# Optimization experiments

Hardware: AMD Instinct MI355X
Metric: run time of the kernel (lower is better)

The kernel has to match this reference:

```python
import jax, jax.numpy as jnp
import numpy as np

B, V, C, CD, D, H, W = 1, 3, 32, 8, 32, 128, 160
LAMB = 1.5


def _bilinear(img, x, y):
    # img: [c, Hs, Ws]; x, y: pixel coords [D, HW]; zero padding, align_corners=True semantics
    c, Hs, Ws = img.shape
    x0 = jnp.floor(x)
    y0 = jnp.floor(y)
    x0i = x0.astype(jnp.int32)
    y0i = y0.astype(jnp.int32)
    wx = x - x0
    wy = y - y0
    imgf = img.reshape(c, Hs * Ws)

    def gather(xi, yi, w):
        valid = (xi >= 0) & (xi < Ws) & (yi >= 0) & (yi < Hs)
        lin = jnp.clip(yi, 0, Hs - 1) * Ws + jnp.clip(xi, 0, Ws - 1)
        v = jnp.take(imgf, lin.reshape(-1), axis=1).reshape((c,) + xi.shape)
        return v * (w * valid.astype(w.dtype))[None]

    return (gather(x0i, y0i, (1 - wx) * (1 - wy))
            + gather(x0i + 1, y0i, wx * (1 - wy))
            + gather(x0i, y0i + 1, (1 - wx) * wy)
            + gather(x0i + 1, y0i + 1, wx * wy))


def _homo_warp(src_fea, src_proj, ref_proj, depth_values):
    # src_fea [B,c,Hs,Ws]; projs [B,4,4]; depth_values [B,D,H,W] -> [B,c,D,H,W]
    b, c, Hs, Ws = src_fea.shape
    _, d, h, w = depth_values.shape
    proj = jnp.einsum('bij,bjk->bik', src_proj, jnp.linalg.inv(ref_proj))
    rot = proj[:, :3, :3]
    tr = proj[:, :3, 3]
    ys, xs = jnp.meshgrid(jnp.arange(h, dtype=src_fea.dtype), jnp.arange(w, dtype=src_fea.dtype), indexing='ij')
    xyz = jnp.stack([xs.reshape(-1), ys.reshape(-1), jnp.ones(h * w, dtype=src_fea.dtype)], 0)  # [3,HW]
    rx = jnp.einsum('bij,jn->bin', rot, xyz)  # [B,3,HW]
    dvals = depth_values.reshape(b, 1, d, h * w)
    pxyz = rx[:, :, None, :] * dvals + tr[:, :, None, None]  # [B,3,D,HW]
    z = pxyz[:, 2]
    px = pxyz[:, 0] / z  # [B,D,HW]
    py = pxyz[:, 1] / z
    out = jax.vmap(_bilinear)(src_fea, px, py)  # [B,c,D,HW]
    return out.reshape(b, c, d, h, w)


def setup_inputs() -> dict:
    key = jax.random.key(0)
    k1, k2, k3 = jax.random.split(key, 3)
    features = jax.random.normal(k1, (V, B, C, H, W), jnp.float32)
    deps_feature_stage = jax.random.normal(k2, (V, B, CD, H, W), jnp.float32)
    reg_w = jax.random.normal(k3, (1, C + CD), jnp.float32) * 0.1
    K = np.array([[200., 0., W / 2.], [0., 200., H / 2.], [0., 0., 1.]])
    mats = []
    for tx in [0.0, 1.0, -1.0]:
        Rt = np.eye(4)
        Rt[0, 3] = tx
        P = np.eye(4)
        P[:3, :4] = K @ Rt[:3, :4]
        mats.append(P)
    proj_matrices = jnp.asarray(np.stack(mats)[None], jnp.float32)  # [B,V,4,4]
    depth_values = jnp.broadcast_to(
        jnp.linspace(5.0, 10.0, D, dtype=jnp.float32)[None, :, None, None], (B, D, H, W)) + jnp.zeros((B, D, H, W), jnp.float32)
    return {'features': features, 'deps_feature_stage': deps_feature_stage,
            'proj_matrices': proj_matrices, 'depth_values': depth_values,
            'reg_w': reg_w, 'num_depth': D, 'stage_idx': 0}


def reference(features, deps_feature_stage, proj_matrices, depth_values, reg_w, num_depth, stage_idx):
    num_views = features.shape[0]
    d = depth_values.shape[1]
    ref_proj = proj_matrices[:, 0]

    def variance_volume(feats):
        ref = feats[0]  # [B,c,H,W]
        ref_vol = jnp.broadcast_to(ref[:, :, None], (ref.shape[0], ref.shape[1], d, ref.shape[2], ref.shape[3]))
        s = ref_vol
        sq = ref_vol * ref_vol
        for v in range(1, num_views):
            wv = _homo_warp(feats[v], proj_matrices[:, v], ref_proj, depth_values)
            s = s + wv
            sq = sq + wv * wv
        return sq / num_views - (s / num_views) ** 2

    volume_variance = variance_volume(features)      # [B,C,D,H,W]
    deps_variance = variance_volume(deps_feature_stage)  # [B,CD,D,H,W]
    var = jnp.concatenate([volume_variance, deps_variance], axis=1)
    # cost_regularization modeled as 1x1x1 conv reducing channels to 1
    cost = jnp.einsum('bcdhw,oc->bodhw', var, reg_w)[:, 0]  # [B,D,H,W]
    prob_volume = jax.nn.softmax(cost, axis=1)
    depth = jnp.sum(prob_volume * depth_values, axis=1)  # [B,H,W]
    samp_variance = (depth_values - depth[:, None]) ** 2
    exp_variance = LAMB * jnp.sqrt(jnp.sum(samp_variance * prob_volume, axis=1))
    return depth, exp_variance, prob_volume
```

## Files before the change

kernel.cpp:

```cpp
#include <hip/hip_runtime.h>
#include <math.h>

#define HH   128
#define WW   160
#define HWN  (HH*WW)
#define NCF  32
#define NCD  8
#define ND   32
#define NV   3
#define LAMBF 1.5f

__global__ __launch_bounds__(256) void prep_k(const float* __restrict__ feat,
                                              const float* __restrict__ deps,
                                              const float* __restrict__ proj,
                                              float* __restrict__ featT,
                                              float* __restrict__ depsT,
                                              float* __restrict__ projw) {
    if (blockIdx.x == 0 && blockIdx.y == 0 && blockIdx.z == 0 && threadIdx.x == 0) {
        float M00 = proj[0], M01 = proj[1], M02 = proj[2],  m0 = proj[3];
        float M10 = proj[4], M11 = proj[5], M12 = proj[6],  m1 = proj[7];
        float M20 = proj[8], M21 = proj[9], M22 = proj[10], m2 = proj[11];
        float c00 =  (M11*M22 - M12*M21);
        float c01 = -(M10*M22 - M12*M20);
        float c02 =  (M10*M21 - M11*M20);
        float det = M00*c00 + M01*c01 + M02*c02;
        float id  = 1.f / det;
        float i00 = c00*id, i01 = -(M01*M22 - M02*M21)*id, i02 =  (M01*M12 - M02*M11)*id;
        float i10 = c01*id, i11 =  (M00*M22 - M02*M20)*id, i12 = -(M00*M12 - M02*M10)*id;
        float i20 = c02*id, i21 = -(M00*M21 - M01*M20)*id, i22 =  (M00*M11 - M01*M10)*id;
        float t0 = -(i00*m0 + i01*m1 + i02*m2);
        float t1 = -(i10*m0 + i11*m1 + i12*m2);
        float t2 = -(i20*m0 + i21*m1 + i22*m2);
        #pragma unroll
        for (int v = 1; v < NV; v++) {
            const float* S = proj + v*16;
            float s00 = S[0], s01 = S[1], s02 = S[2],  st0 = S[3];
            float s10 = S[4], s11 = S[5], s12 = S[6],  st1 = S[7];
            float s20 = S[8], s21 = S[9], s22 = S[10], st2 = S[11];
            float* o = projw + (v-1)*12;
            o[0] = s00*i00 + s01*i10 + s02*i20;
            o[1] = s00*i01 + s01*i11 + s02*i21;
            o[2] = s00*i02 + s01*i12 + s02*i22;
            o[3] = s10*i00 + s11*i10 + s12*i20;
            o[4] = s10*i01 + s11*i11 + s12*i21;
            o[5] = s10*i02 + s11*i12 + s12*i22;
            o[6] = s20*i00 + s21*i10 + s22*i20;
            o[7] = s20*i01 + s21*i11 + s22*i21;
            o[8] = s20*i02 + s21*i12 + s22*i22;
            o[9]  = s00*t0 + s01*t1 + s02*t2 + st0;
            o[10] = s10*t0 + s11*t1 + s12*t2 + st1;
            o[11] = s20*t0 + s21*t1 + s22*t2 + st2;
        }
    }

    __shared__ float lds[NCF][33];
    const int z  = blockIdx.z;
    const int xb = blockIdx.x * 32;
    const int y  = blockIdx.y;
    const float* src;
    float*       dst;
    int CH;
    if (z < NV) {
        CH = NCF;
        src = feat + (size_t)(z*NCF)*HWN + y*WW + xb;
        dst = featT + (size_t)(z*HWN + y*WW + xb) * NCF;
    } else {
        CH = NCD;
        src = deps + (size_t)((z - NV)*NCD)*HWN + y*WW + xb;
        dst = depsT + (size_t)((z - NV)*HWN + y*WW + xb) * NCD;
    }
    for (int i = threadIdx.x; i < CH*32; i += 256) {
        int c = i >> 5, xl = i & 31;
        lds[c][xl] = src[c*HWN + xl];
    }
    __syncthreads();
    for (int i = threadIdx.x; i < CH*32; i += 256) {
        int c = i % CH, xl = i / CH;
        dst[i] = lds[c][xl];
    }
}

__global__ __launch_bounds__(256) void cost_volume_k(
    const float* __restrict__ featT,
    const float* __restrict__ depsT,
    const float* __restrict__ dvals,
    const float* __restrict__ regw,
    const float* __restrict__ pws,
    float* __restrict__ out)
{
    __shared__ float cl [ND][9];
    __shared__ float dvl[ND][9];
    __shared__ float smax[8], sisum[8];

    const int t    = threadIdx.x;
    const int lane = t & 63;
    const int wid  = t >> 6;
    const int cg   = lane & 7;
    const int pl   = lane >> 3;
    const int pixg = blockIdx.x * 8 + pl;
    const int y    = pixg / WW;
    const int x    = pixg - y * WW;
    const float fx = (float)x, fy = (float)y;
    const int dbase = wid * 8;

    float RX[2], RY[2], RZ[2], T0[2], T1[2], T2[2];
    #pragma unroll
    for (int v = 0; v < 2; v++) {
        const float* q = pws + v*12;
        RX[v] = q[0]*fx + q[1]*fy + q[2];
        RY[v] = q[3]*fx + q[4]*fy + q[5];
        RZ[v] = q[6]*fx + q[7]*fy + q[8];
        T0[v] = q[9]; T1[v] = q[10]; T2[v] = q[11];
    }

    {
        float4 r4 = *(const float4*)(featT + (size_t)pixg*NCF + cg*4);
        float4 w4 = *(const float4*)(regw + cg*4);
        const float wca0 = w4.x*(1.f/3.f), wca1 = w4.y*(1.f/3.f),
                    wca2 = w4.z*(1.f/3.f), wca3 = w4.w*(1.f/3.f);
        const float wcb0 = w4.x*(1.f/9.f), wcb1 = w4.y*(1.f/9.f),
                    wcb2 = w4.z*(1.f/9.f), wcb3 = w4.w*(1.f/9.f);
        const float rx0 = r4.x, rx1 = r4.y, rx2 = r4.z, rx3 = r4.w;
        const float* b1 = featT + (size_t)1*HWN*NCF;
        const float* b2 = featT + (size_t)2*HWN*NCF;
        const int cg4 = cg*4;

        #pragma unroll 2
        for (int jj = 0; jj < 8; jj++) {
            const int d = dbase + jj;
            float dvv = dvals[d*HWN + pixg];
            if (cg == 0) dvl[d][pl] = dvv;

            float s0 = rx0, s1 = rx1, s2 = rx2, s3 = rx3;
            float q0 = rx0*rx0, q1 = rx1*rx1, q2 = rx2*rx2, q3 = rx3*rx3;

            #pragma unroll
            for (int v = 0; v < 2; v++) {
                float pz = RZ[v]*dvv + T2[v];
                float iz = __builtin_amdgcn_rcpf(pz);
                float px = (RX[v]*dvv + T0[v]) * iz;
                float py = (RY[v]*dvv + T1[v]) * iz;
                float x0f = floorf(px), y0f = floorf(py);
                int x0 = (int)x0f, y0 = (int)y0f;
                float wx = px - x0f, wy = py - y0f;
                float omx = 1.f - wx, omy = 1.f - wy;
                bool vx0 = (x0 >= 0) & (x0 < WW);
                bool vx1 = (x0+1 >= 0) & (x0+1 < WW);
                bool vy0 = (y0 >= 0) & (y0 < HH);
                bool vy1 = (y0+1 >= 0) & (y0+1 < HH);
                float W00 = (vx0 && vy0) ? omx*omy : 0.f;
                float W10 = (vx1 && vy0) ? wx*omy  : 0.f;
                float W01 = (vx0 && vy1) ? omx*wy  : 0.f;
                float W11 = (vx1 && vy1) ? wx*wy   : 0.f;
                int xc0 = min(max(x0,   0), WW-1);
                int xc1 = min(max(x0+1, 0), WW-1);
                int yc0 = min(max(y0,   0), HH-1);
                int yc1 = min(max(y0+1, 0), HH-1);
                const float* b = v ? b2 : b1;
                int o00 = (yc0*WW + xc0)*NCF + cg4;
                int o10 = (yc0*WW + xc1)*NCF + cg4;
                int o01 = (yc1*WW + xc0)*NCF + cg4;
                int o11 = (yc1*WW + xc1)*NCF + cg4;
                float4 f00 = *(const float4*)(b + o00);
                float4 f10 = *(const float4*)(b + o10);
                float4 f01 = *(const float4*)(b + o01);
                float4 f11 = *(const float4*)(b + o11);
                float wv0 = W00*f00.x + W10*f10.x + W01*f01.x + W11*f11.x;
                float wv1 = W00*f00.y + W10*f10.y + W01*f01.y + W11*f11.y;
                float wv2 = W00*f00.z + W10*f10.z + W01*f01.z + W11*f11.z;
                float wv3 = W00*f00.w + W10*f10.w + W01*f01.w + W11*f11.w;
                s0 += wv0; q0 = fmaf(wv0, wv0, q0);
                s1 += wv1; q1 = fmaf(wv1, wv1, q1);
                s2 += wv2; q2 = fmaf(wv2, wv2, q2);
                s3 += wv3; q3 = fmaf(wv3, wv3, q3);
            }
            float part = wca0*q0 - wcb0*s0*s0;
            part = fmaf(wca1, q1, part); part = fmaf(-wcb1, s1*s1, part);
            part = fmaf(wca2, q2, part); part = fmaf(-wcb2, s2*s2, part);
            part = fmaf(wca3, q3, part); part = fmaf(-wcb3, s3*s3, part);
            part += __shfl_xor(part, 1);
            part += __shfl_xor(part, 2);
            part += __shfl_xor(part, 4);
            if (cg == 0) cl[d][pl] = part;
        }
    }
    __syncthreads();

    {
        const int cgd  = lane & 1;
        const int dsub = (lane >> 1) & 3;
        float4 r4 = *(const float4*)(depsT + (size_t)pixg*NCD + cgd*4);
        float4 w4 = *(const float4*)(regw + NCF + cgd*4);
        const float wca0 = w4.x*(1.f/3.f), wca1 = w4.y*(1.f/3.f),
                    wca2 = w4.z*(1.f/3.f), wca3 = w4.w*(1.f/3.f);
        const float wcb0 = w4.x*(1.f/9.f), wcb1 = w4.y*(1.f/9.f),
                    wcb2 = w4.z*(1.f/9.f), wcb3 = w4.w*(1.f/9.f);
        const float rx0 = r4.x, rx1 = r4.y, rx2 = r4.z, rx3 = r4.w;
        const float* b1 = depsT + (size_t)1*HWN*NCD;
        const float* b2 = depsT + (size_t)2*HWN*NCD;
        const int cg4 = cgd*4;

        #pragma unroll
        for (int i = 0; i < 2; i++) {
            const int d = dbase + dsub + 4*i;
            float dvv = dvl[d][pl];

            float s0 = rx0, s1 = rx1, s2 = rx2, s3 = rx3;
            float q0 = rx0*rx0, q1 = rx1*rx1, q2 = rx2*rx2, q3 = rx3*rx3;

            #pragma unroll
            for (int v = 0; v < 2; v++) {
                float pz = RZ[v]*dvv + T2[v];
                float iz = __builtin_amdgcn_rcpf(pz);
                float px = (RX[v]*dvv + T0[v]) * iz;
                float py = (RY[v]*dvv + T1[v]) * iz;
                float x0f = floorf(px), y0f = floorf(py);
                int x0 = (int)x0f, y0 = (int)y0f;
                float wx = px - x0f, wy = py - y0f;
                float omx = 1.f - wx, omy = 1.f - wy;
                bool vx0 = (x0 >= 0) & (x0 < WW);
                bool vx1 = (x0+1 >= 0) & (x0+1 < WW);
                bool vy0 = (y0 >= 0) & (y0 < HH);
                bool vy1 = (y0+1 >= 0) & (y0+1 < HH);
                float W00 = (vx0 && vy0) ? omx*omy : 0.f;
                float W10 = (vx1 && vy0) ? wx*omy  : 0.f;
                float W01 = (vx0 && vy1) ? omx*wy  : 0.f;
                float W11 = (vx1 && vy1) ? wx*wy   : 0.f;
                int xc0 = min(max(x0,   0), WW-1);
                int xc1 = min(max(x0+1, 0), WW-1);
                int yc0 = min(max(y0,   0), HH-1);
                int yc1 = min(max(y0+1, 0), HH-1);
                const float* b = v ? b2 : b1;
                int o00 = (yc0*WW + xc0)*NCD + cg4;
                int o10 = (yc0*WW + xc1)*NCD + cg4;
                int o01 = (yc1*WW + xc0)*NCD + cg4;
                int o11 = (yc1*WW + xc1)*NCD + cg4;
                float4 f00 = *(const float4*)(b + o00);
                float4 f10 = *(const float4*)(b + o10);
                float4 f01 = *(const float4*)(b + o01);
                float4 f11 = *(const float4*)(b + o11);
                float wv0 = W00*f00.x + W10*f10.x + W01*f01.x + W11*f11.x;
                float wv1 = W00*f00.y + W10*f10.y + W01*f01.y + W11*f11.y;
                float wv2 = W00*f00.z + W10*f10.z + W01*f01.z + W11*f11.z;
                float wv3 = W00*f00.w + W10*f10.w + W01*f01.w + W11*f11.w;
                s0 += wv0; q0 = fmaf(wv0, wv0, q0);
                s1 += wv1; q1 = fmaf(wv1, wv1, q1);
                s2 += wv2; q2 = fmaf(wv2, wv2, q2);
                s3 += wv3; q3 = fmaf(wv3, wv3, q3);
            }
            float part = wca0*q0 - wcb0*s0*s0;
            part = fmaf(wca1, q1, part); part = fmaf(-wcb1, s1*s1, part);
            part = fmaf(wca2, q2, part); part = fmaf(-wcb2, s2*s2, part);
            part = fmaf(wca3, q3, part); part = fmaf(-wcb3, s3*s3, part);
            part += __shfl_xor(part, 1);
            if (cgd == 0) cl[d][pl] += part;
        }
    }
    __syncthreads();

    if (t < 8) {
        const int plx  = t;
        const int pixo = blockIdx.x * 8 + plx;
        float m = -1e30f;
        #pragma unroll
        for (int d = 0; d < ND; d++) m = fmaxf(m, cl[d][plx]);
        float sum = 0.f, pd = 0.f, pd2 = 0.f;
        #pragma unroll
        for (int d = 0; d < ND; d++) {
            float e   = __expf(cl[d][plx] - m);
            float dvv = dvl[d][plx];
            sum += e;
            pd  = fmaf(e, dvv, pd);
            pd2 = fmaf(e, dvv*dvv, pd2);
        }
        float isum  = 1.f / sum;
        float depth = pd * isum;
        float sv    = pd2 * isum - depth*depth;
        float ev    = LAMBF * sqrtf(fmaxf(sv, 0.f));
        smax[plx]  = m;
        sisum[plx] = isum;
        out[pixo]       = depth;
        out[HWN + pixo] = ev;
    }
    __syncthreads();
    {
        const int plx  = t & 7;
        const int dd   = t >> 3;
        const int pixo = blockIdx.x * 8 + plx;
        out[2*HWN + dd*HWN + pixo] = __expf(cl[dd][plx] - smax[plx]) * sisum[plx];
    }
}

extern "C" void kernel_launch(void* const* d_in, const int* in_sizes, int n_in,
                              void* d_out, int out_size, void* d_ws, size_t ws_size,
                              hipStream_t stream) {
    const float* features = (const float*)d_in[0];
    const float* deps     = (const float*)d_in[1];
    const float* proj     = (const float*)d_in[2];
    const float* dvals    = (const float*)d_in[3];
    const float* regw     = (const float*)d_in[4];

    float* ws    = (float*)d_ws;
    float* projw = ws;
    float* featT = ws + 64;
    float* depsT = featT + (size_t)NV*HWN*NCF;

    dim3 tg(WW/32, HH, 2*NV);
    prep_k<<<tg, 256, 0, stream>>>(features, deps, proj, featT, depsT, projw);

    cost_volume_k<<<HWN/8, 256, 0, stream>>>(featT, depsT, dvals, regw, projw,
                                             (float*)d_out);
}
```

Measured before the change: 106.3 us.

## Share bilinear setup across channel lanes via shuffles and vectorize transpose

In the main feature pass, each of the 8 channel-group lanes of a pixel now computes the projection and bilinear weights and offsets for one depth, instead of all 8 lanes repeating the same math for every depth. The results are broadcast with wave shuffles inside the depth loop. This cuts redundant ALU work, such as reciprocals, floors and clamps, at the cost of 16 shuffles per depth iteration. Separately, the prep transpose now uses float4 loads and stores through LDS to reduce memory instruction count.

Measured after the change: 103.9 us. -2.3%, faster.

```diff
diff --git a/kernel.cpp b/kernel.cpp
--- a/kernel.cpp
+++ b/kernel.cpp
@@ -9,6 +9,21 @@
 #define ND   32
 #define NV   3
 #define LAMBF 1.5f
+
+template <int CH>
+__device__ void transpose_tile(const float* __restrict__ src, float* __restrict__ dst,
+                               float (*lds)[33], int tid) {
+    for (int i = tid; i < CH*8; i += 256) {
+        int c = i >> 3, xg = (i & 7) << 2;
+        *(float4*)&lds[c][xg] = *(const float4*)(src + c*HWN + xg);
+    }
+    __syncthreads();
+    for (int i = tid; i < 32*(CH/4); i += 256) {
+        int xl = i / (CH/4), c4 = (i % (CH/4)) * 4;
+        float4 t = make_float4(lds[c4][xl], lds[c4+1][xl], lds[c4+2][xl], lds[c4+3][xl]);
+        *(float4*)(dst + xl*CH + c4) = t;
+    }
+}
 
 __global__ __launch_bounds__(256) void prep_k(const float* __restrict__ feat,
                                               const float* __restrict__ deps,
@@ -57,26 +72,14 @@
     const int z  = blockIdx.z;
     const int xb = blockIdx.x * 32;
     const int y  = blockIdx.y;
-    const float* src;
-    float*       dst;
-    int CH;
     if (z < NV) {
-        CH = NCF;
-        src = feat + (size_t)(z*NCF)*HWN + y*WW + xb;
-        dst = featT + (size_t)(z*HWN + y*WW + xb) * NCF;
+        transpose_tile<NCF>(feat + (size_t)(z*NCF)*HWN + y*WW + xb,
+                            featT + (size_t)(z*HWN + y*WW + xb) * NCF,
+                            lds, threadIdx.x);
     } else {
-        CH = NCD;
-        src = deps + (size_t)((z - NV)*NCD)*HWN + y*WW + xb;
-        dst = depsT + (size_t)((z - NV)*HWN + y*WW + xb) * NCD;
-    }
-    for (int i = threadIdx.x; i < CH*32; i += 256) {
-        int c = i >> 5, xl = i & 31;
-        lds[c][xl] = src[c*HWN + xl];
-    }
-    __syncthreads();
-    for (int i = threadIdx.x; i < CH*32; i += 256) {
-        int c = i % CH, xl = i / CH;
-        dst[i] = lds[c][xl];
+        transpose_tile<NCD>(deps + (size_t)((z - NV)*NCD)*HWN + y*WW + xb,
+                            depsT + (size_t)((z - NV)*HWN + y*WW + xb) * NCD,
+                            lds, threadIdx.x);
     }
 }
 
@@ -113,7 +116,45 @@
         T0[v] = q[9]; T1[v] = q[10]; T2[v] = q[11];
     }
 
+    auto bsetup = [&](float dvv, int v, int CH, float& w00, float& w10,
+                      float& w01, float& w11, int& o00, int& o10,
+                      int& o01, int& o11) {
+        float pz = RZ[v]*dvv + T2[v];
+        float iz = __builtin_amdgcn_rcpf(pz);
+        float px = (RX[v]*dvv + T0[v]) * iz;
+        float py = (RY[v]*dvv + T1[v]) * iz;
+        float x0f = floorf(px), y0f = floorf(py);
+        int x0 = (int)x0f, y0 = (int)y0f;
+        float wx = px - x0f, wy = py - y0f;
+        float omx = 1.f - wx, omy = 1.f - wy;
+        bool vx0 = (x0 >= 0) & (x0 < WW);
+        bool vx1 = (x0+1 >= 0) & (x0+1 < WW);
+        bool vy0 = (y0 >= 0) & (y0 < HH);
+        bool vy1 = (y0+1 >= 0) & (y0+1 < HH);
+        w00 = (vx0 && vy0) ? omx*omy : 0.f;
+        w10 = (vx1 && vy0) ? wx*omy  : 0.f;
+        w01 = (vx0 && vy1) ? omx*wy  : 0.f;
+        w11 = (vx1 && vy1) ? wx*wy   : 0.f;
+        int xc0 = min(max(x0,   0), WW-1);
+        int xc1 = min(max(x0+1, 0), WW-1);
+        int yc0 = min(max(y0,   0), HH-1);
+        int yc1 = min(max(y0+1, 0), HH-1);
+        o00 = (yc0*WW + xc0)*CH;
+        o10 = (yc0*WW + xc1)*CH;
+        o01 = (yc1*WW + xc0)*CH;
+        o11 = (yc1*WW + xc1)*CH;
+    };
+
     {
+        float dvv_own = dvals[(dbase + cg)*HWN + pixg];
+        dvl[dbase + cg][pl] = dvv_own;
+        float SW00[2], SW10[2], SW01[2], SW11[2];
+        int   SO00[2], SO10[2], SO01[2], SO11[2];
+        #pragma unroll
+        for (int v = 0; v < 2; v++)
+            bsetup(dvv_own, v, NCF, SW00[v], SW10[v], SW01[v], SW11[v],
+                   SO00[v], SO10[v], SO01[v], SO11[v]);
+
         float4 r4 = *(const float4*)(featT + (size_t)pixg*NCF + cg*4);
         float4 w4 = *(const float4*)(regw + cg*4);
         const float wca0 = w4.x*(1.f/3.f), wca1 = w4.y*(1.f/3.f),
@@ -121,46 +162,27 @@
         const float wcb0 = w4.x*(1.f/9.f), wcb1 = w4.y*(1.f/9.f),
                     wcb2 = w4.z*(1.f/9.f), wcb3 = w4.w*(1.f/9.f);
         const float rx0 = r4.x, rx1 = r4.y, rx2 = r4.z, rx3 = r4.w;
-        const float* b1 = featT + (size_t)1*HWN*NCF;
-        const float* b2 = featT + (size_t)2*HWN*NCF;
-        const int cg4 = cg*4;
+        const float* b1 = featT + (size_t)1*HWN*NCF + cg*4;
+        const float* b2 = featT + (size_t)2*HWN*NCF + cg*4;
+        const int plbase = lane & 0x38;
 
         #pragma unroll 2
         for (int jj = 0; jj < 8; jj++) {
-            const int d = dbase + jj;
-            float dvv = dvals[d*HWN + pixg];
-            if (cg == 0) dvl[d][pl] = dvv;
-
+            const int src = plbase | jj;
             float s0 = rx0, s1 = rx1, s2 = rx2, s3 = rx3;
             float q0 = rx0*rx0, q1 = rx1*rx1, q2 = rx2*rx2, q3 = rx3*rx3;
 
             #pragma unroll
             for (int v = 0; v < 2; v++) {
-                float pz = RZ[v]*dvv + T2[v];
-                float iz = __builtin_amdgcn_rcpf(pz);
-                float px = (RX[v]*dvv + T0[v]) * iz;
-                float py = (RY[v]*dvv + T1[v]) * iz;
-                float x0f = floorf(px), y0f = floorf(py);
-                int x0 = (int)x0f, y0 = (int)y0f;
-                float wx = px - x0f, wy = py - y0f;
-                float omx = 1.f - wx, omy = 1.f - wy;
-                bool vx0 = (x0 >= 0) & (x0 < WW);
-                bool vx1 = (x0+1 >= 0) & (x0+1 < WW);
-                bool vy0 = (y0 >= 0) & (y0 < HH);
-                bool vy1 = (y0+1 >= 0) & (y0+1 < HH);
-                float W00 = (vx0 && vy0) ? omx*omy : 0.f;
-                float W10 = (vx1 && vy0) ? wx*omy  : 0.f;
-                float W01 = (vx0 && vy1) ? omx*wy  : 0.f;
-                float W11 = (vx1 && vy1) ? wx*wy   : 0.f;
-                int xc0 = min(max(x0,   0), WW-1);
-                int xc1 = min(max(x0+1, 0), WW-1);
-                int yc0 = min(max(y0,   0), HH-1);
-                int yc1 = min(max(y0+1, 0), HH-1);
+                float W00 = __shfl(SW00[v], src, 64);
+                float W10 = __shfl(SW10[v], src, 64);
+                float W01 = __shfl(SW01[v], src, 64);
+                float W11 = __shfl(SW11[v], src, 64);
+                int   o00 = __shfl(SO00[v], src, 64);
+                int   o10 = __shfl(SO10[v], src, 64);
+                int   o01 = __shfl(SO01[v], src, 64);
+                int   o11 = __shfl(SO11[v], src, 64);
                 const float* b = v ? b2 : b1;
-                int o00 = (yc0*WW + xc0)*NCF + cg4;
-                int o10 = (yc0*WW + xc1)*NCF + cg4;
-                int o01 = (yc1*WW + xc0)*NCF + cg4;
-                int o11 = (yc1*WW + xc1)*NCF + cg4;
                 float4 f00 = *(const float4*)(b + o00);
                 float4 f10 = *(const float4*)(b + o10);
                 float4 f01 = *(const float4*)(b + o01);
@@ -181,7 +203,7 @@
             part += __shfl_xor(part, 1);
             part += __shfl_xor(part, 2);
             part += __shfl_xor(part, 4);
-            if (cg == 0) cl[d][pl] = part;
+            if (cg == jj) cl[dbase + jj][pl] = part;
         }
     }
     __syncthreads();
@@ -196,45 +218,21 @@
         const float wcb0 = w4.x*(1.f/9.f), wcb1 = w4.y*(1.f/9.f),
                     wcb2 = w4.z*(1.f/9.f), wcb3 = w4.w*(1.f/9.f);
         const float rx0 = r4.x, rx1 = r4.y, rx2 = r4.z, rx3 = r4.w;
-        const float* b1 = depsT + (size_t)1*HWN*NCD;
-        const float* b2 = depsT + (size_t)2*HWN*NCD;
-        const int cg4 = cgd*4;
+        const float* b1 = depsT + (size_t)1*HWN*NCD + cgd*4;
+        const float* b2 = depsT + (size_t)2*HWN*NCD + cgd*4;
 
         #pragma unroll
         for (int i = 0; i < 2; i++) {
             const int d = dbase + dsub + 4*i;
             float dvv = dvl[d][pl];
-
             float s0 = rx0, s1 = rx1, s2 = rx2, s3 = rx3;
             float q0 = rx0*rx0, q1 = rx1*rx1, q2 = rx2*rx2, q3 = rx3*rx3;
 
             #pragma unroll
             for (int v = 0; v < 2; v++) {
-                float pz = RZ[v]*dvv + T2[v];
-                float iz = __builtin_amdgcn_rcpf(pz);
-                float px = (RX[v]*dvv + T0[v]) * iz;
-                float py = (RY[v]*dvv + T1[v]) * iz;
-                float x0f = floorf(px), y0f = floorf(py);
-                int x0 = (int)x0f, y0 = (int)y0f;
-                float wx = px - x0f, wy = py - y0f;
-                float omx = 1.f - wx, omy = 1.f - wy;
-                bool vx0 = (x0 >= 0) & (x0 < WW);
-                bool vx1 = (x0+1 >= 0) & (x0+1 < WW);
-                bool vy0 = (y0 >= 0) & (y0 < HH);
-                bool vy1 = (y0+1 >= 0) & (y0+1 < HH);
-                float W00 = (vx0 && vy0) ? omx*omy : 0.f;
-                float W10 = (vx1 && vy0) ? wx*omy  : 0.f;
-                float W01 = (vx0 && vy1) ? omx*wy  : 0.f;
-                float W11 = (vx1 && vy1) ? wx*wy   : 0.f;
-                int xc0 = min(max(x0,   0), WW-1);
-                int xc1 = min(max(x0+1, 0), WW-1);
-                int yc0 = min(max(y0,   0), HH-1);
-                int yc1 = min(max(y0+1, 0), HH-1);
+                float W00, W10, W01, W11; int o00, o10, o01, o11;
+                bsetup(dvv, v, NCD, W00, W10, W01, W11, o00, o10, o01, o11);
                 const float* b = v ? b2 : b1;
-                int o00 = (yc0*WW + xc0)*NCD + cg4;
-                int o10 = (yc0*WW + xc1)*NCD + cg4;
-                int o01 = (yc1*WW + xc0)*NCD + cg4;
-                int o11 = (yc1*WW + xc1)*NCD + cg4;
                 float4 f00 = *(const float4*)(b + o00);
                 float4 f10 = *(const float4*)(b + o10);
                 float4 f01 = *(const float4*)(b + o01);
```
